# Kernel optimization log

Hardware: AMD Instinct MI355X
Metric: run time of the kernel (lower is better)

## Reference

```python
import jax, jax.numpy as jnp
import numpy as np

N_NODES = 8192
IN_FEATS, H_FEATS, NUM_CLASSES = 512, 256, 16


def _glorot(key, shape):
    fan_in, fan_out = shape[0], shape[1]
    limit = float(np.sqrt(6.0 / (fan_in + fan_out)))
    return jax.random.uniform(key, shape, jnp.float32, -limit, limit)


def setup_inputs() -> dict:
    key = jax.random.key(0)
    ks = jax.random.split(key, 16)
    return {
        "x": jax.random.normal(ks[0], (N_NODES, IN_FEATS), jnp.float32),
        "w1": _glorot(ks[1], (IN_FEATS, H_FEATS)), "b1": jnp.zeros((H_FEATS,), jnp.float32),
        "w2": _glorot(ks[2], (H_FEATS, H_FEATS)), "b2": jnp.zeros((H_FEATS,), jnp.float32),
        "w3": _glorot(ks[3], (H_FEATS, 32)),      "b3": jnp.zeros((32,), jnp.float32),
        "t": _glorot(ks[4], (1, 1)), "theta": _glorot(ks[5], (1, 1)),
        "gw1": _glorot(ks[6], (32, 16)), "gb1": jnp.zeros((16,), jnp.float32),
        "gw2": _glorot(ks[7], (16, 8)),  "gb2": jnp.zeros((8,), jnp.float32),
        "lw1": _glorot(ks[8], (8, 16)),  "lb1": jnp.zeros((16,), jnp.float32),
        "lw2": _glorot(ks[9], (16, NUM_CLASSES)), "lb2": jnp.zeros((NUM_CLASSES,), jnp.float32),
    }


def _pairwise_dist(h):
    # Euclidean cdist(h, h): [N, N], stable sqrt with zero subgradient at d=0
    sq = jnp.sum(h * h, axis=1)
    d2 = jnp.maximum(sq[:, None] + sq[None, :] - 2.0 * (h @ h.T), 0.0)
    return jnp.where(d2 > 0.0, jnp.sqrt(jnp.where(d2 > 0.0, d2, 1.0)), 0.0)


def reference(x, w1, b1, w2, b2, w3, b3, t, theta, gw1, gb1, gw2, gb2, lw1, lb1, lw2, lb2):
    n = x.shape[0]
    # MLP encoder (dropout is eval-mode identity)
    h = jax.nn.relu(x @ w1 + b1)
    h = jax.nn.relu(h @ w2 + b2)
    h = h @ w3 + b3                                  # [N, 32]
    # latent dense graph: A = sigmoid(t * (cdist + theta)); all entries > 0 -> fully dense graph
    A = jax.nn.sigmoid(t[0, 0] * (_pairwise_dist(h) + theta[0, 0]))   # [N, N]
    inv_deg = 1.0 / n                                # norm='right', in-degree == N for dense graph
    # GraphConv: dst aggregates sum_src A[src,dst] * (h[src] @ W) then right-normalizes
    h = jax.nn.relu((A.T @ (h @ gw1)) * inv_deg + gb1)   # [N, 16]
    h = jax.nn.relu((A.T @ (h @ gw2)) * inv_deg + gb2)   # [N, 8]
    h = jax.nn.relu(h @ lw1 + lb1)
    return h @ lw2 + lb2                             # [N, num_classes]
```

## Files before the change

### kernel.cpp

```cpp
#include <hip/hip_runtime.h>

typedef __attribute__((ext_vector_type(8))) short short8;
typedef __attribute__((ext_vector_type(4))) float f32x4;
typedef __attribute__((ext_vector_type(2))) unsigned int u32x2;
typedef unsigned short u16;
typedef unsigned int u32;

#define MFMA16 __builtin_amdgcn_mfma_f32_16x16x32_bf16

constexpr int NCH = 16;
constexpr int NJT = 8192 / 64 / NCH;

__device__ __forceinline__ void lds_order_fence() { asm volatile("" ::: "memory"); }

__device__ __forceinline__ u16 f2bf(float f) {
    u32 u = __builtin_bit_cast(u32, f);
    return (u16)((u + 0x7FFFu + ((u >> 16) & 1u)) >> 16);
}

__device__ __forceinline__ void split2(float f, u16& hi, u16& lo) {
    u32 u = __builtin_bit_cast(u32, f);
    hi = (u16)(u >> 16);
    float hf = __builtin_bit_cast(float, u & 0xFFFF0000u);
    float r = f - hf;
    lo = (u16)(__builtin_bit_cast(u32, r) >> 16);
}

__device__ __forceinline__ int swzA(int row, int slot) {
    return row * 64 + ((slot ^ ((row >> 1) & 3)) << 4);
}

__global__ void __launch_bounds__(256) k_trs_all(const float* __restrict__ w1, u16* __restrict__ wt1h,
                                                 u16* __restrict__ wt1l,
                                                 const float* __restrict__ w2, u16* __restrict__ wt2h,
                                                 u16* __restrict__ wt2l,
                                                 const float* __restrict__ w3, u16* __restrict__ wt3h,
                                                 u16* __restrict__ wt3l) {
    const int idx = blockIdx.x * 256 + threadIdx.x;
    float v;
    int off;
    u16 *ph, *pl;
    if (idx < 131072) {
        const int k = idx >> 8, n = idx & 255;
        v = w1[idx];
        off = n * 512 + k;
        ph = wt1h; pl = wt1l;
    } else if (idx < 196608) {
        const int i2 = idx - 131072;
        const int k = i2 >> 8, n = i2 & 255;
        v = w2[i2];
        off = n * 256 + k;
        ph = wt2h; pl = wt2l;
    } else {
        const int i3 = idx - 196608;
        const int k = i3 >> 5, n = i3 & 31;
        v = w3[i3];
        off = n * 256 + k;
        ph = wt3h; pl = wt3l;
    }
    u16 hh, ll;
    split2(v, hh, ll);
    ph[off] = hh;
    pl[off] = ll;
}

template <int K, int BN, bool RELU, bool AF32, bool OUTSPLIT>
__global__ void __launch_bounds__(256, 2) k_gemm(const float* __restrict__ Af,
                                                 const u16* __restrict__ Ahi,
                                                 const u16* __restrict__ Alo,
                                                 const u16* __restrict__ Bthi,
                                                 const u16* __restrict__ Btlo,
                                                 const float* __restrict__ bias,
                                                 float* __restrict__ Cf, u16* __restrict__ Chi,
                                                 u16* __restrict__ Clo, const int N) {
    constexpr int NT = BN / 16;
    __shared__ __align__(16) char smem[16384];
    char* const Ah = smem;
    char* const Al = smem + 4096;
    char* const Bh = smem + 8192;
    char* const Bl = smem + 12288;
    const int tid = threadIdx.x, lane = tid & 63, w = tid >> 6;
    const int frow = lane & 15, fg = lane >> 4;
    const int m0 = blockIdx.x * 64, n0 = blockIdx.y * BN;
    const int srow = tid >> 2, sc = tid & 3;
    const int swa = swzA(srow, sc);
    const bool doB = (BN == 64) || (tid < 128);
    const float* gA = AF32 ? (Af + (m0 + srow) * K + sc * 8) : nullptr;
    const u16* gAh = AF32 ? nullptr : (Ahi + (m0 + srow) * K + sc * 8);
    const u16* gAl = AF32 ? nullptr : (Alo + (m0 + srow) * K + sc * 8);
    const u16* gBh = Bthi + (n0 + srow) * K + sc * 8;
    const u16* gBl = Btlo + (n0 + srow) * K + sc * 8;

    f32x4 acc[NT];
    float bv[NT];
#pragma unroll
    for (int nt = 0; nt < NT; nt++) {
        acc[nt] = {0.f, 0.f, 0.f, 0.f};
        bv[nt] = bias[n0 + nt * 16 + frow];
    }
    const int fra = swzA(w * 16 + frow, fg);
    int frb[NT];
#pragma unroll
    for (int nt = 0; nt < NT; nt++) frb[nt] = swzA(nt * 16 + frow, fg);

    for (int k0 = 0; k0 < K; k0 += 32) {
        short8 ah8, al8, bh8, bl8;
        if constexpr (AF32) {
            const f32x4 a0 = *(const f32x4*)(gA + k0);
            const f32x4 a1 = *(const f32x4*)(gA + k0 + 4);
#pragma unroll
            for (int i = 0; i < 4; i++) { u16 hh, ll; split2(a0[i], hh, ll); ah8[i] = (short)hh; al8[i] = (short)ll; }
#pragma unroll
            for (int i = 0; i < 4; i++) { u16 hh, ll; split2(a1[i], hh, ll); ah8[4 + i] = (short)hh; al8[4 + i] = (short)ll; }
        } else {
            ah8 = *(const short8*)(gAh + k0);
            al8 = *(const short8*)(gAl + k0);
        }
        if (doB) {
            bh8 = *(const short8*)(gBh + k0);
            bl8 = *(const short8*)(gBl + k0);
        }
        __syncthreads();
        *(short8*)(Ah + swa) = ah8;
        *(short8*)(Al + swa) = al8;
        if (doB) {
            *(short8*)(Bh + swa) = bh8;
            *(short8*)(Bl + swa) = bl8;
        }
        __syncthreads();
        const short8 afh = *(const short8*)(Ah + fra);
        const short8 afl = *(const short8*)(Al + fra);
#pragma unroll
        for (int nt = 0; nt < NT; nt++) {
            const short8 bfh = *(const short8*)(Bh + frb[nt]);
            const short8 bfl = *(const short8*)(Bl + frb[nt]);
            acc[nt] = MFMA16(afh, bfh, acc[nt], 0, 0, 0);
            acc[nt] = MFMA16(afh, bfl, acc[nt], 0, 0, 0);
            acc[nt] = MFMA16(afl, bfh, acc[nt], 0, 0, 0);
        }
    }
#pragma unroll
    for (int nt = 0; nt < NT; nt++) {
#pragma unroll
        for (int r = 0; r < 4; r++) {
            float v = acc[nt][r] + bv[nt];
            if (RELU) v = fmaxf(v, 0.f);
            const int row = m0 + w * 16 + fg * 4 + r, col = n0 + nt * 16 + frow;
            if constexpr (OUTSPLIT) {
                u16 hh, ll;
                split2(v, hh, ll);
                Chi[row * N + col] = hh;
                Clo[row * N + col] = ll;
            } else {
                Cf[row * N + col] = v;
            }
        }
    }
}

__global__ void __launch_bounds__(256) k_post(const float* __restrict__ H,
                                              const float* __restrict__ gw1,
                                              u16* __restrict__ hhi, u16* __restrict__ hlo,
                                              float* __restrict__ sqv, u16* __restrict__ B1t) {
    __shared__ float gs[512];
    const int tid = threadIdx.x;
    gs[tid] = gw1[tid];
    gs[tid + 256] = gw1[tid + 256];
    __syncthreads();
    const int j = blockIdx.x * 256 + tid;
    float h[32];
#pragma unroll
    for (int q = 0; q < 8; q++) {
        f32x4 v = *(const f32x4*)(H + j * 32 + q * 4);
        h[q * 4 + 0] = v[0]; h[q * 4 + 1] = v[1]; h[q * 4 + 2] = v[2]; h[q * 4 + 3] = v[3];
    }
    float s = 0.f;
#pragma unroll
    for (int k = 0; k < 32; k++) s = fmaf(h[k], h[k], s);
    sqv[j] = s;
#pragma unroll
    for (int q = 0; q < 4; q++) {
        short8 vh, vl;
#pragma unroll
        for (int e = 0; e < 8; e++) {
            u16 hh, ll;
            split2(h[q * 8 + e], hh, ll);
            vh[e] = (short)hh; vl[e] = (short)ll;
        }
        *(short8*)(hhi + j * 32 + q * 8) = vh;
        *(short8*)(hlo + j * 32 + q * 8) = vl;
    }
    const float inv = 0.0001220703125f;
#pragma unroll
    for (int f = 0; f < 16; f++) {
        float a = 0.f;
#pragma unroll
        for (int k = 0; k < 32; k++) a = fmaf(h[k], gs[k * 16 + f], a);
        B1t[f * 8192 + j] = f2bf(a * inv);
    }
}

template <bool DIAG>
__device__ __forceinline__ void ew_pack(char* astr, int awoff, const f32x4 s, const f32x4 sq4,
                                        float sq_i, float c0, float c1, int jloc, int il) {
    float p[4];
#pragma unroll
    for (int r = 0; r < 4; r++) {
        float d2 = fmaf(s[r], -2.f, sq_i + sq4[r]);
        d2 = fmaxf(d2, 0.f);
        float d = __builtin_amdgcn_sqrtf(d2);
        if (DIAG) {
            if (jloc + r == il) d = 0.f;
        }
        const float z = fmaf(d, c1, c0);
        p[r] = __builtin_amdgcn_rcpf(1.f + __builtin_amdgcn_exp2f(z));
    }
    u32 w0, w1;
    asm("v_cvt_pk_bf16_f32 %0, %1, %2" : "=v"(w0) : "v"(p[0]), "v"(p[1]));
    asm("v_cvt_pk_bf16_f32 %0, %1, %2" : "=v"(w1) : "v"(p[2]), "v"(p[3]));
    u32x2 pk = {w0, w1};
    *(u32x2*)(astr + awoff) = pk;
}

__global__ void __launch_bounds__(512) k_agg(const u16* __restrict__ hhi, const u16* __restrict__ hlo,
                                             const float* __restrict__ sqv, const u16* __restrict__ Bt,
                                             float* __restrict__ P,
                                             const float* __restrict__ tp, const float* __restrict__ thp) {
    __shared__ __align__(16) char smem[32768];
    char* const bufh = smem;
    char* const bufl = smem + 8192;
    char* const astr0 = smem + 16384;

    const int tid = threadIdx.x, lane = tid & 63, w = tid >> 6;
    const int frow = lane & 15, fg = lane >> 4;
    const int dstbase = blockIdx.x * 128;
    const int chunk = blockIdx.y;
    const float t = tp[0], th = thp[0];
    const float c1 = -t * 1.44269504088896340736f;
    const float c0 = c1 * th;
    char* const astr = astr0 + w * 2048;

    const bool stager = (tid < 256);
    const int srow = (tid & 255) >> 2, sc = tid & 3;
    const int swa = swzA(srow, sc);

    const int igf = dstbase + w * 16 + frow;
    const short8 hdh = *(const short8*)(hhi + igf * 32 + fg * 8);
    const short8 hdl = *(const short8*)(hlo + igf * 32 + fg * 8);
    const float sq_i = sqv[igf];
    const int jdiag = dstbase + ((w >> 2) << 6);
    const int il = (w & 3) * 16 + frow;

    int awo[4], ard[2];
#pragma unroll
    for (int jj = 0; jj < 4; jj++)
        awo[jj] = frow * 128 + (((2 * jj + (fg >> 1)) ^ (frow & 7)) << 4) + ((fg & 1) << 3);
#pragma unroll
    for (int h = 0; h < 2; h++) ard[h] = frow * 128 + (((4 * h + fg) ^ (frow & 7)) << 4);

    f32x4 outacc = {0.f, 0.f, 0.f, 0.f};
    const u16* bgp = Bt + frow * 8192;

    const int jt0 = chunk * NJT;
    short8 pvh, pvl;
    if (stager) {
        pvh = *(const short8*)(hhi + ((jt0 * 64) + srow) * 32 + sc * 8);
        pvl = *(const short8*)(hlo + ((jt0 * 64) + srow) * 32 + sc * 8);
        *(short8*)(bufh + swa) = pvh;
        *(short8*)(bufl + swa) = pvl;
        if (NJT > 1) {
            const int jn = (jt0 + 1) * 64;
            pvh = *(const short8*)(hhi + (jn + srow) * 32 + sc * 8);
            pvl = *(const short8*)(hlo + (jn + srow) * 32 + sc * 8);
        }
    }

    for (int it = 0; it < NJT; ++it) {
        const int b = it & 1;
        const int jbase = (jt0 + it) * 64;
        f32x4 sqg[4];
        short8 bfg[2];
#pragma unroll
        for (int q = 0; q < 4; q++) sqg[q] = *(const f32x4*)(sqv + jbase + q * 16 + fg * 4);
#pragma unroll
        for (int q = 0; q < 2; q++) bfg[q] = *(const short8*)(bgp + jbase + q * 32 + fg * 8);
        __syncthreads();
        if (stager) {
            if (it + 1 < NJT) {
                *(short8*)(bufh + (b ^ 1) * 4096 + swa) = pvh;
                *(short8*)(bufl + (b ^ 1) * 4096 + swa) = pvl;
            }
            if (it + 2 < NJT) {
                const int jn = (jt0 + it + 2) * 64;
                pvh = *(const short8*)(hhi + (jn + srow) * 32 + sc * 8);
                pvl = *(const short8*)(hlo + (jn + srow) * 32 + sc * 8);
            }
        }
        char* const bh = bufh + b * 4096;
        char* const bl = bufl + b * 4096;
        const bool diag = (jbase == jdiag);
#pragma unroll
        for (int h = 0; h < 2; ++h) {
            const short8 hs0h = *(const short8*)(bh + swzA(h * 32 + frow, fg));
            const short8 hs0l = *(const short8*)(bl + swzA(h * 32 + frow, fg));
            const short8 hs1h = *(const short8*)(bh + swzA(h * 32 + 16 + frow, fg));
            const short8 hs1l = *(const short8*)(bl + swzA(h * 32 + 16 + frow, fg));
            f32x4 s0 = {0.f, 0.f, 0.f, 0.f}, s1 = {0.f, 0.f, 0.f, 0.f};
            s0 = MFMA16(hs0h, hdh, s0, 0, 0, 0);
            s0 = MFMA16(hs0h, hdl, s0, 0, 0, 0);
            s0 = MFMA16(hs0l, hdh, s0, 0, 0, 0);
            s1 = MFMA16(hs1h, hdh, s1, 0, 0, 0);
            s1 = MFMA16(hs1h, hdl, s1, 0, 0, 0);
            s1 = MFMA16(hs1l, hdh, s1, 0, 0, 0);
            lds_order_fence();
            if (diag) {
                ew_pack<true>(astr, awo[2 * h], s0, sqg[2 * h], sq_i, c0, c1, (2 * h) * 16 + fg * 4, il);
                ew_pack<true>(astr, awo[2 * h + 1], s1, sqg[2 * h + 1], sq_i, c0, c1, (2 * h + 1) * 16 + fg * 4, il);
            } else {
                ew_pack<false>(astr, awo[2 * h], s0, sqg[2 * h], sq_i, c0, c1, 0, -1);
                ew_pack<false>(astr, awo[2 * h + 1], s1, sqg[2 * h + 1], sq_i, c0, c1, 0, -1);
            }
            lds_order_fence();
            const short8 af = *(const short8*)(astr + ard[h]);
            outacc = MFMA16(af, bfg[h], outacc, 0, 0, 0);
        }
    }
#pragma unroll
    for (int r = 0; r < 4; r++) {
        const int ig = dstbase + w * 16 + fg * 4 + r;
        P[(chunk * 8192 + ig) * 16 + frow] = outacc[r];
    }
}

__global__ void __launch_bounds__(256) k_reduce1(const float* __restrict__ P,
                                                 const float* __restrict__ gw2,
                                                 const float* __restrict__ gb1,
                                                 u16* __restrict__ B2t) {
    __shared__ float gs[128];
    const int tid = threadIdx.x;
    if (tid < 128) gs[tid] = gw2[tid];
    __syncthreads();
    const int j = blockIdx.x * 256 + tid;
    float g[16];
#pragma unroll
    for (int q = 0; q < 4; q++) {
        f32x4 v = *(const f32x4*)(P + j * 16 + q * 4);
        g[q * 4 + 0] = v[0]; g[q * 4 + 1] = v[1]; g[q * 4 + 2] = v[2]; g[q * 4 + 3] = v[3];
    }
#pragma unroll
    for (int c = 1; c < NCH; c++) {
#pragma unroll
        for (int q = 0; q < 4; q++) {
            f32x4 v = *(const f32x4*)(P + (c * 8192 + j) * 16 + q * 4);
            g[q * 4 + 0] += v[0]; g[q * 4 + 1] += v[1]; g[q * 4 + 2] += v[2]; g[q * 4 + 3] += v[3];
        }
    }
#pragma unroll
    for (int f = 0; f < 16; f++) g[f] = fmaxf(g[f] + gb1[f], 0.f);
    const float inv = 0.0001220703125f;
#pragma unroll
    for (int f2 = 0; f2 < 8; f2++) {
        float a = 0.f;
#pragma unroll
        for (int k = 0; k < 16; k++) a = fmaf(g[k], gs[k * 8 + f2], a);
        B2t[f2 * 8192 + j] = f2bf(a * inv);
    }
#pragma unroll
    for (int f2 = 8; f2 < 16; f2++) B2t[f2 * 8192 + j] = 0;
}

__global__ void __launch_bounds__(256) k_final(const float* __restrict__ P,
                                               const float* __restrict__ gb2,
                                               const float* __restrict__ lw1,
                                               const float* __restrict__ lb1,
                                               const float* __restrict__ lw2,
                                               const float* __restrict__ lb2,
                                               float* __restrict__ out) {
    __shared__ float s1[128], s2[256];
    const int tid = threadIdx.x;
    if (tid < 128) s1[tid] = lw1[tid];
    s2[tid] = lw2[tid];
    __syncthreads();
    const int j = blockIdx.x * 256 + tid;
    float g[8];
#pragma unroll
    for (int q = 0; q < 2; q++) {
        f32x4 v = *(const f32x4*)(P + j * 16 + q * 4);
        g[q * 4 + 0] = v[0]; g[q * 4 + 1] = v[1]; g[q * 4 + 2] = v[2]; g[q * 4 + 3] = v[3];
    }
#pragma unroll
    for (int c = 1; c < NCH; c++) {
#pragma unroll
        for (int q = 0; q < 2; q++) {
            f32x4 v = *(const f32x4*)(P + (c * 8192 + j) * 16 + q * 4);
            g[q * 4 + 0] += v[0]; g[q * 4 + 1] += v[1]; g[q * 4 + 2] += v[2]; g[q * 4 + 3] += v[3];
        }
    }
#pragma unroll
    for (int f = 0; f < 8; f++) g[f] = fmaxf(g[f] + gb2[f], 0.f);
    float l1[16];
#pragma unroll
    for (int f = 0; f < 16; f++) {
        float a = lb1[f];
#pragma unroll
        for (int k = 0; k < 8; k++) a = fmaf(g[k], s1[k * 16 + f], a);
        l1[f] = fmaxf(a, 0.f);
    }
#pragma unroll
    for (int q = 0; q < 4; q++) {
        f32x4 v;
#pragma unroll
        for (int e = 0; e < 4; e++) {
            const int f = q * 4 + e;
            float a = lb2[f];
#pragma unroll
            for (int k = 0; k < 16; k++) a = fmaf(l1[k], s2[k * 16 + f], a);
            v[e] = a;
        }
        *(f32x4*)(out + j * 16 + q * 4) = v;
    }
}

extern "C" void kernel_launch(void* const* d_in, const int* in_sizes, int n_in,
                              void* d_out, int out_size, void* d_ws, size_t ws_size,
                              hipStream_t stream) {
    (void)in_sizes; (void)n_in; (void)out_size; (void)ws_size;
    const float* x   = (const float*)d_in[0];
    const float* w1  = (const float*)d_in[1];
    const float* b1  = (const float*)d_in[2];
    const float* w2  = (const float*)d_in[3];
    const float* b2  = (const float*)d_in[4];
    const float* w3  = (const float*)d_in[5];
    const float* b3  = (const float*)d_in[6];
    const float* t   = (const float*)d_in[7];
    const float* th  = (const float*)d_in[8];
    const float* gw1 = (const float*)d_in[9];
    const float* gb1 = (const float*)d_in[10];
    const float* gw2 = (const float*)d_in[11];
    const float* gb2 = (const float*)d_in[12];
    const float* lw1 = (const float*)d_in[13];
    const float* lb1 = (const float*)d_in[14];
    const float* lw2 = (const float*)d_in[15];
    const float* lb2 = (const float*)d_in[16];

    char* ws = (char*)d_ws;
    u16* wt1h = (u16*)(ws + 0);
    u16* wt1l = (u16*)(ws + 262144);
    u16* wt2h = (u16*)(ws + 524288);
    u16* wt2l = (u16*)(ws + 655360);
    u16* wt3h = (u16*)(ws + 786432);
    u16* wt3l = (u16*)(ws + 802816);
    u16* H1h  = (u16*)(ws + 819200);
    u16* H1l  = (u16*)(ws + 5013504);
    float* P  = (float*)(ws + 819200);
    u16* H2h  = (u16*)(ws + 9207808);
    u16* H2l  = (u16*)(ws + 13402112);
    float* H  = (float*)(ws + 17596416);
    u16*   hhi = (u16*)(ws + 18644992);
    u16*   hlo = (u16*)(ws + 19169280);
    float* sqv = (float*)(ws + 19693568);
    u16*   B1t = (u16*)(ws + 19726336);
    u16*   B2t = (u16*)(ws + 19988480);

    k_trs_all<<<800, 256, 0, stream>>>(w1, wt1h, wt1l, w2, wt2h, wt2l, w3, wt3h, wt3l);

    k_gemm<512, 64, true, true, true><<<dim3(128, 4), 256, 0, stream>>>(
        x, nullptr, nullptr, wt1h, wt1l, b1, nullptr, H1h, H1l, 256);
    k_gemm<256, 64, true, false, true><<<dim3(128, 4), 256, 0, stream>>>(
        nullptr, H1h, H1l, wt2h, wt2l, b2, nullptr, H2h, H2l, 256);
    k_gemm<256, 32, false, false, false><<<dim3(128, 1), 256, 0, stream>>>(
        nullptr, H2h, H2l, wt3h, wt3l, b3, H, nullptr, nullptr, 32);

    k_post<<<32, 256, 0, stream>>>(H, gw1, hhi, hlo, sqv, B1t);

    k_agg<<<dim3(64, NCH), 512, 0, stream>>>(hhi, hlo, sqv, B1t, P, t, th);
    k_reduce1<<<32, 256, 0, stream>>>(P, gw2, gb1, B2t);
    k_agg<<<dim3(64, NCH), 512, 0, stream>>>(hhi, hlo, sqv, B2t, P, t, th);
    k_final<<<32, 256, 0, stream>>>(P, gb2, lw1, lb1, lw2, lb2, (float*)d_out);
}
```

Before: 131.2 us.

## Load source-node fragments directly into registers in aggregation kernel, dropping LDS staging

The aggregation kernel no longer stages source-node hi/lo features through double-buffered shared memory with a block-wide barrier each tile. Each wave now loads its MFMA operand fragments straight from global memory into registers and prefetches the next tile one step ahead. Blocks shrink from 512 to 256 threads covering 64 destination rows, so the grid doubles and LDS use drops to the per-wave probability scratch. The goal is to remove per-tile __syncthreads and LDS traffic, at the cost of redundant global/L2 reads of source features across waves and more registers per thread.

```diff
diff --git a/kernel.cpp b/kernel.cpp
--- a/kernel.cpp
+++ b/kernel.cpp
@@ -222,34 +222,26 @@
     *(u32x2*)(astr + awoff) = pk;
 }
 
-__global__ void __launch_bounds__(512) k_agg(const u16* __restrict__ hhi, const u16* __restrict__ hlo,
+__global__ void __launch_bounds__(256) k_agg(const u16* __restrict__ hhi, const u16* __restrict__ hlo,
                                              const float* __restrict__ sqv, const u16* __restrict__ Bt,
                                              float* __restrict__ P,
                                              const float* __restrict__ tp, const float* __restrict__ thp) {
-    __shared__ __align__(16) char smem[32768];
-    char* const bufh = smem;
-    char* const bufl = smem + 8192;
-    char* const astr0 = smem + 16384;
+    __shared__ __align__(16) char astr0[8192];
 
     const int tid = threadIdx.x, lane = tid & 63, w = tid >> 6;
     const int frow = lane & 15, fg = lane >> 4;
-    const int dstbase = blockIdx.x * 128;
+    const int dstbase = blockIdx.x * 64;
     const int chunk = blockIdx.y;
     const float t = tp[0], th = thp[0];
     const float c1 = -t * 1.44269504088896340736f;
     const float c0 = c1 * th;
     char* const astr = astr0 + w * 2048;
 
-    const bool stager = (tid < 256);
-    const int srow = (tid & 255) >> 2, sc = tid & 3;
-    const int swa = swzA(srow, sc);
-
     const int igf = dstbase + w * 16 + frow;
     const short8 hdh = *(const short8*)(hhi + igf * 32 + fg * 8);
     const short8 hdl = *(const short8*)(hlo + igf * 32 + fg * 8);
     const float sq_i = sqv[igf];
-    const int jdiag = dstbase + ((w >> 2) << 6);
-    const int il = (w & 3) * 16 + frow;
+    const int il = w * 16 + frow;
 
     int awo[4], ard[2];
 #pragma unroll
@@ -260,51 +252,39 @@
 
     f32x4 outacc = {0.f, 0.f, 0.f, 0.f};
     const u16* bgp = Bt + frow * 8192;
-
     const int jt0 = chunk * NJT;
-    short8 pvh, pvl;
-    if (stager) {
-        pvh = *(const short8*)(hhi + ((jt0 * 64) + srow) * 32 + sc * 8);
-        pvl = *(const short8*)(hlo + ((jt0 * 64) + srow) * 32 + sc * 8);
-        *(short8*)(bufh + swa) = pvh;
-        *(short8*)(bufl + swa) = pvl;
-        if (NJT > 1) {
-            const int jn = (jt0 + 1) * 64;
-            pvh = *(const short8*)(hhi + (jn + srow) * 32 + sc * 8);
-            pvl = *(const short8*)(hlo + (jn + srow) * 32 + sc * 8);
-        }
-    }
-
+
+    short8 ch[4], cl[4];
+#pragma unroll
+    for (int q = 0; q < 4; q++) {
+        const int row = jt0 * 64 + q * 16 + frow;
+        ch[q] = *(const short8*)(hhi + row * 32 + fg * 8);
+        cl[q] = *(const short8*)(hlo + row * 32 + fg * 8);
+    }
+
+#pragma unroll
     for (int it = 0; it < NJT; ++it) {
-        const int b = it & 1;
         const int jbase = (jt0 + it) * 64;
+        short8 nh[4], nl[4];
+        if (it + 1 < NJT) {
+#pragma unroll
+            for (int q = 0; q < 4; q++) {
+                const int row = jbase + 64 + q * 16 + frow;
+                nh[q] = *(const short8*)(hhi + row * 32 + fg * 8);
+                nl[q] = *(const short8*)(hlo + row * 32 + fg * 8);
+            }
+        }
         f32x4 sqg[4];
         short8 bfg[2];
 #pragma unroll
         for (int q = 0; q < 4; q++) sqg[q] = *(const f32x4*)(sqv + jbase + q * 16 + fg * 4);
 #pragma unroll
         for (int q = 0; q < 2; q++) bfg[q] = *(const short8*)(bgp + jbase + q * 32 + fg * 8);
-        __syncthreads();
-        if (stager) {
-            if (it + 1 < NJT) {
-                *(short8*)(bufh + (b ^ 1) * 4096 + swa) = pvh;
-                *(short8*)(bufl + (b ^ 1) * 4096 + swa) = pvl;
-            }
-            if (it + 2 < NJT) {
-                const int jn = (jt0 + it + 2) * 64;
-                pvh = *(const short8*)(hhi + (jn + srow) * 32 + sc * 8);
-                pvl = *(const short8*)(hlo + (jn + srow) * 32 + sc * 8);
-            }
-        }
-        char* const bh = bufh + b * 4096;
-        char* const bl = bufl + b * 4096;
-        const bool diag = (jbase == jdiag);
+        const bool diag = (jbase == dstbase);
 #pragma unroll
         for (int h = 0; h < 2; ++h) {
-            const short8 hs0h = *(const short8*)(bh + swzA(h * 32 + frow, fg));
-            const short8 hs0l = *(const short8*)(bl + swzA(h * 32 + frow, fg));
-            const short8 hs1h = *(const short8*)(bh + swzA(h * 32 + 16 + frow, fg));
-            const short8 hs1l = *(const short8*)(bl + swzA(h * 32 + 16 + frow, fg));
+            const short8 hs0h = ch[h * 2], hs0l = cl[h * 2];
+            const short8 hs1h = ch[h * 2 + 1], hs1l = cl[h * 2 + 1];
             f32x4 s0 = {0.f, 0.f, 0.f, 0.f}, s1 = {0.f, 0.f, 0.f, 0.f};
             s0 = MFMA16(hs0h, hdh, s0, 0, 0, 0);
             s0 = MFMA16(hs0h, hdl, s0, 0, 0, 0);
@@ -323,6 +303,10 @@
             lds_order_fence();
             const short8 af = *(const short8*)(astr + ard[h]);
             outacc = MFMA16(af, bfg[h], outacc, 0, 0, 0);
+        }
+        if (it + 1 < NJT) {
+#pragma unroll
+            for (int q = 0; q < 4; q++) { ch[q] = nh[q]; cl[q] = nl[q]; }
         }
     }
 #pragma unroll
@@ -473,8 +457,8 @@
 
     k_post<<<32, 256, 0, stream>>>(H, gw1, hhi, hlo, sqv, B1t);
 
-    k_agg<<<dim3(64, NCH), 512, 0, stream>>>(hhi, hlo, sqv, B1t, P, t, th);
+    k_agg<<<dim3(128, NCH), 256, 0, stream>>>(hhi, hlo, sqv, B1t, P, t, th);
     k_reduce1<<<32, 256, 0, stream>>>(P, gw2, gb1, B2t);
-    k_agg<<<dim3(64, NCH), 512, 0, stream>>>(hhi, hlo, sqv, B2t, P, t, th);
+    k_agg<<<dim3(128, NCH), 256, 0, stream>>>(hhi, hlo, sqv, B2t, P, t, th);
     k_final<<<32, 256, 0, stream>>>(P, gb2, lw1, lb1, lw2, lb2, (float*)d_out);
 }
```

New measurement: 170.6 us. 1.3x slower.

## Materialize bf16 adjacency in first aggregation and reuse it in second

Applied to the files above, without the earlier changes.

The first aggregation pass now writes the bf16 sigmoid adjacency fragments (8192x8192, 128 MB) to workspace. A new lightweight kernel then runs the second aggregation as a plain MFMA GEMM over the stored fragments. This removes the recomputation of pairwise distances, sqrt, exp and rcp in the second pass. In exchange it adds a 128 MB write and a 128 MB read of HBM traffic, and it only takes effect when the workspace is large enough.

```diff
diff --git a/kernel.cpp b/kernel.cpp
--- a/kernel.cpp
+++ b/kernel.cpp
@@ -222,9 +222,10 @@
     *(u32x2*)(astr + awoff) = pk;
 }
 
+template <bool STOREA>
 __global__ void __launch_bounds__(512) k_agg(const u16* __restrict__ hhi, const u16* __restrict__ hlo,
                                              const float* __restrict__ sqv, const u16* __restrict__ Bt,
-                                             float* __restrict__ P,
+                                             float* __restrict__ P, u16* __restrict__ Afr,
                                              const float* __restrict__ tp, const float* __restrict__ thp) {
     __shared__ __align__(16) char smem[32768];
     char* const bufh = smem;
@@ -239,6 +240,7 @@
     const float c1 = -t * 1.44269504088896340736f;
     const float c0 = c1 * th;
     char* const astr = astr0 + w * 2048;
+    const int dfi = blockIdx.x * 8 + w;
 
     const bool stager = (tid < 256);
     const int srow = (tid & 255) >> 2, sc = tid & 3;
@@ -322,8 +324,41 @@
             }
             lds_order_fence();
             const short8 af = *(const short8*)(astr + ard[h]);
+            if (STOREA) {
+                *(short8*)(Afr + (dfi * 128 + (jt0 + it)) * 1024 + lane * 16 + h * 8) = af;
+            }
             outacc = MFMA16(af, bfg[h], outacc, 0, 0, 0);
         }
+    }
+#pragma unroll
+    for (int r = 0; r < 4; r++) {
+        const int ig = dstbase + w * 16 + fg * 4 + r;
+        P[(chunk * 8192 + ig) * 16 + frow] = outacc[r];
+    }
+}
+
+__global__ void __launch_bounds__(512) k_agg2(const u16* __restrict__ Afr, const u16* __restrict__ Bt,
+                                              float* __restrict__ P) {
+    const int tid = threadIdx.x, lane = tid & 63, w = tid >> 6;
+    const int frow = lane & 15, fg = lane >> 4;
+    const int dstbase = blockIdx.x * 128;
+    const int chunk = blockIdx.y;
+    const int dfi = blockIdx.x * 8 + w;
+    const u16* bgp = Bt + frow * 8192;
+    const int jt0 = chunk * NJT;
+
+    f32x4 outacc = {0.f, 0.f, 0.f, 0.f};
+#pragma unroll
+    for (int it = 0; it < NJT; ++it) {
+        const int sti = jt0 + it;
+        const int jbase = sti * 64;
+        const u16* ap = Afr + (dfi * 128 + sti) * 1024 + lane * 16;
+        const short8 af0 = *(const short8*)(ap);
+        const short8 af1 = *(const short8*)(ap + 8);
+        const short8 bf0 = *(const short8*)(bgp + jbase + fg * 8);
+        const short8 bf1 = *(const short8*)(bgp + jbase + 32 + fg * 8);
+        outacc = MFMA16(af0, bf0, outacc, 0, 0, 0);
+        outacc = MFMA16(af1, bf1, outacc, 0, 0, 0);
     }
 #pragma unroll
     for (int r = 0; r < 4; r++) {
@@ -424,7 +459,7 @@
 extern "C" void kernel_launch(void* const* d_in, const int* in_sizes, int n_in,
                               void* d_out, int out_size, void* d_ws, size_t ws_size,
                               hipStream_t stream) {
-    (void)in_sizes; (void)n_in; (void)out_size; (void)ws_size;
+    (void)in_sizes; (void)n_in; (void)out_size;
     const float* x   = (const float*)d_in[0];
     const float* w1  = (const float*)d_in[1];
     const float* b1  = (const float*)d_in[2];
@@ -461,6 +496,8 @@
     float* sqv = (float*)(ws + 19693568);
     u16*   B1t = (u16*)(ws + 19726336);
     u16*   B2t = (u16*)(ws + 19988480);
+    u16*   Afr = (u16*)(ws + 20971520);
+    const bool bigws = ws_size >= (20971520ull + 134217728ull);
 
     k_trs_all<<<800, 256, 0, stream>>>(w1, wt1h, wt1l, w2, wt2h, wt2l, w3, wt3h, wt3l);
 
@@ -473,8 +510,14 @@
 
     k_post<<<32, 256, 0, stream>>>(H, gw1, hhi, hlo, sqv, B1t);
 
-    k_agg<<<dim3(64, NCH), 512, 0, stream>>>(hhi, hlo, sqv, B1t, P, t, th);
-    k_reduce1<<<32, 256, 0, stream>>>(P, gw2, gb1, B2t);
-    k_agg<<<dim3(64, NCH), 512, 0, stream>>>(hhi, hlo, sqv, B2t, P, t, th);
+    if (bigws) {
+        k_agg<true><<<dim3(64, NCH), 512, 0, stream>>>(hhi, hlo, sqv, B1t, P, Afr, t, th);
+        k_reduce1<<<32, 256, 0, stream>>>(P, gw2, gb1, B2t);
+        k_agg2<<<dim3(64, NCH), 512, 0, stream>>>(Afr, B2t, P);
+    } else {
+        k_agg<false><<<dim3(64, NCH), 512, 0, stream>>>(hhi, hlo, sqv, B1t, P, nullptr, t, th);
+        k_reduce1<<<32, 256, 0, stream>>>(P, gw2, gb1, B2t);
+        k_agg<false><<<dim3(64, NCH), 512, 0, stream>>>(hhi, hlo, sqv, B2t, P, nullptr, t, th);
+    }
     k_final<<<32, 256, 0, stream>>>(P, gb2, lw1, lb1, lw2, lb2, (float*)d_out);
 }
```

After: 124.9 us. 1.05x faster.
